# Optimization experiments

Hardware: AMD Instinct MI355X
Metric: run time of the kernel (lower is better)

## Reference

```python
import jax, jax.numpy as jnp
import numpy as np

S, B, H, NH = 2048, 4, 1024, 16
HD = H // NH
MASK_VAL = -10000.0

def setup_inputs() -> dict:
    key = jax.random.key(0)
    ks = jax.random.split(key, 6)
    hidden_states = jax.random.normal(ks[0], (S, B, H), dtype=jnp.float32)
    attention_mask = jax.random.randint(ks[1], (B, 1, S, S), 0, 2).astype(bool)
    W_qkv = jax.random.normal(ks[2], (3 * H, H), dtype=jnp.float32) * (H ** -0.5)
    b_qkv = jax.random.normal(ks[3], (3 * H,), dtype=jnp.float32) * 0.02
    W_dense = jax.random.normal(ks[4], (H, H), dtype=jnp.float32) * (H ** -0.5)
    b_dense = jax.random.normal(ks[5], (H,), dtype=jnp.float32) * 0.02
    return {"hidden_states": hidden_states, "attention_mask": attention_mask,
            "W_qkv": W_qkv, "b_qkv": b_qkv, "W_dense": W_dense, "b_dense": b_dense}

def reference(hidden_states, attention_mask, W_qkv, b_qkv, W_dense, b_dense):
    # QKV projection: [s,b,h] -> [s,b,3h] -> [s,b,NH,3*HD], split last dim into q,k,v
    mixed = hidden_states @ W_qkv.T + b_qkv
    mixed = mixed.reshape(S, B, NH, 3 * HD)
    q, k, v = mixed[..., :HD], mixed[..., HD:2 * HD], mixed[..., 2 * HD:]
    norm_factor = jnp.float32(1.0 / np.sqrt(HD))
    # scores: [b, nh, sq, sk] (baddbmm beta=0.7 on torch.empty is undefined; baseline treated as 0)
    scores = jnp.einsum('sbhd,tbhd->bhst', q, k) * norm_factor
    scores = jnp.where(attention_mask, MASK_VAL, scores)
    probs = jax.nn.softmax(scores, axis=-1)
    # attention dropout (p=0.7) omitted for deterministic reference (eval mode)
    ctx = jnp.einsum('bhst,tbhd->sbhd', probs, v)  # [s,b,nh,hd]
    ctx = ctx.reshape(S, B, H)
    out = ctx @ W_dense.T + b_dense
    return out
```

## Files before the change

### kernel.cpp

```cpp
#include <hip/hip_runtime.h>
#include <hip/hip_bf16.h>
#include <math.h>

constexpr int S_ = 2048, B_ = 4, H_ = 1024, NH_ = 16, HD_ = 64;

typedef __attribute__((ext_vector_type(8))) short short8;
typedef __attribute__((ext_vector_type(4))) short short4v;
typedef __attribute__((ext_vector_type(4))) float floatx4;
typedef __attribute__((ext_vector_type(2))) unsigned uint2v;

static __device__ __forceinline__ short f2bf(float f) {
    union { float f; unsigned u; } v; v.f = f;
    unsigned r = v.u + 0x7FFFu + ((v.u >> 16) & 1u);
    return (short)(r >> 16);
}

static __device__ __forceinline__ unsigned pack_bf(float p0, float p1) {
    return __builtin_amdgcn_perm(__float_as_uint(p1), __float_as_uint(p0), 0x07060302u);
}
static __device__ __forceinline__ float bfl(unsigned u) { return __uint_as_float(u << 16); }
static __device__ __forceinline__ float bfh(unsigned u) { return __uint_as_float(u & 0xFFFF0000u); }

static __device__ __forceinline__ void gl2lds16(const void* g, void* l) {
    __builtin_amdgcn_global_load_lds(
        (const __attribute__((address_space(1))) void*)g,
        (__attribute__((address_space(3))) void*)l, 16, 0, 0);
}

static __device__ __forceinline__ short8 pswz(unsigned a0, unsigned a1,
                                              unsigned b0, unsigned b1) {
    uint2v r0 = __builtin_amdgcn_permlane32_swap(a0, b0, false, false);
    uint2v s0 = __builtin_amdgcn_permlane16_swap(r0.x, r0.y, false, false);
    uint2v r1 = __builtin_amdgcn_permlane32_swap(a1, b1, false, false);
    uint2v s1 = __builtin_amdgcn_permlane16_swap(r1.x, r1.y, false, false);
    union { unsigned u[4]; short8 s; } o;
    o.u[0] = s0.x;
    o.u[1] = s1.x;
    o.u[2] = s0.y;
    o.u[3] = s1.y;
    return o.s;
}

__global__ __launch_bounds__(256) void cvt3_kernel(
    const float* __restrict__ a, short* __restrict__ oa, int na,
    const float* __restrict__ b, short* __restrict__ ob, int nb,
    const float* __restrict__ c, short* __restrict__ oc, int nc)
{
    const int idx = blockIdx.x * 256 + threadIdx.x;
    const float* src; short* dst; int i;
    if (idx < na)            { src = a; dst = oa; i = idx; }
    else if (idx < na + nb)  { src = b; dst = ob; i = idx - na; }
    else                     { src = c; dst = oc; i = idx - na - nb; }
    const float4 v = ((const float4*)src)[i];
    short4v o = { (short)f2bf(v.x), (short)f2bf(v.y), (short)f2bf(v.z), (short)f2bf(v.w) };
    ((short4v*)dst)[i] = o;
}

__global__ __launch_bounds__(256) void mask_u8_kernel(
    const int* __restrict__ m, unsigned* __restrict__ mb)
{
    const int i = blockIdx.x * 256 + threadIdx.x;
    const int4 v = ((const int4*)m)[i];
    unsigned r = (v.x ? 0u : 0xFFu)      | (v.y ? 0u : 0xFF00u) |
                 (v.z ? 0u : 0xFF0000u)  | (v.w ? 0u : 0xFF000000u);
    mb[i] = r;
}

__global__ __launch_bounds__(256) void gemm_qkv_mfma(
    const short* __restrict__ A, const short* __restrict__ Bw,
    const float* __restrict__ bias,
    short* __restrict__ Qb, short* __restrict__ Kb, short* __restrict__ Vb)
{
    constexpr int K = H_;
    __shared__ __align__(16) short As[128 * 64];
    __shared__ __align__(16) short Bs[128 * 64];

    const int t = threadIdx.x;
    const int wave = t >> 6, lane = t & 63;
    const int l15 = lane & 15, quad = lane >> 4;
    const int wm = wave & 1, wn = wave >> 1;
    const int row0 = blockIdx.y * 128;
    const int col0 = blockIdx.x * 128;

    floatx4 acc[4][4];
#pragma unroll
    for (int mi = 0; mi < 4; ++mi)
#pragma unroll
        for (int ni = 0; ni < 4; ++ni)
            acc[mi][ni] = (floatx4){0.f, 0.f, 0.f, 0.f};

    for (int k0 = 0; k0 < K; k0 += 64) {
#pragma unroll
        for (int j = 0; j < 4; ++j) {
            const int c = wave * 256 + j * 64 + lane;
            const int r = c >> 3, jg = ((c & 7) ^ (r & 7)) * 8;
            gl2lds16(A  + (size_t)(row0 + r) * K + k0 + jg, &As[(wave * 256 + j * 64) * 8]);
            gl2lds16(Bw + (size_t)(col0 + r) * K + k0 + jg, &Bs[(wave * 256 + j * 64) * 8]);
        }
        __syncthreads();
#pragma unroll
        for (int kk = 0; kk < 64; kk += 32) {
            short8 af[4], bfr[4];
#pragma unroll
            for (int mi = 0; mi < 4; ++mi) {
                const int R = wm * 64 + mi * 16 + l15;
                af[mi] = *(const short8*)&As[R * 64 + ((((kk >> 3) + quad) ^ (R & 7)) * 8)];
            }
#pragma unroll
            for (int ni = 0; ni < 4; ++ni) {
                const int R = wn * 64 + ni * 16 + l15;
                bfr[ni] = *(const short8*)&Bs[R * 64 + ((((kk >> 3) + quad) ^ (R & 7)) * 8)];
            }
#pragma unroll
            for (int mi = 0; mi < 4; ++mi)
#pragma unroll
                for (int ni = 0; ni < 4; ++ni)
                    acc[mi][ni] = __builtin_amdgcn_mfma_f32_16x16x32_bf16(
                        af[mi], bfr[ni], acc[mi][ni], 0, 0, 0);
        }
        __syncthreads();
    }

#pragma unroll
    for (int ni = 0; ni < 4; ++ni) {
        const int gc = col0 + wn * 64 + ni * 16 + l15;
        const float bv = bias[gc];
        const int hh = gc / 192;
        const int rem = gc - hh * 192;
        const int which = rem >> 6, d = rem & 63;
#pragma unroll
        for (int mi = 0; mi < 4; ++mi)
#pragma unroll
            for (int i = 0; i < 4; ++i) {
                const int gr = row0 + wm * 64 + mi * 16 + quad * 4 + i;
                const int s = gr >> 2, bb = gr & 3;
                float fv = acc[mi][ni][i] + bv;
                const size_t ho = (size_t)(bb * NH_ + hh);
                if (which == 0)      Qb[(ho * S_ + s) * HD_ + d] = f2bf(fv * 0.1803368801111204f);
                else if (which == 1) Kb[(ho * S_ + s) * HD_ + d] = f2bf(fv);
                else                 Vb[(ho * S_ + s) * HD_ + d] = f2bf(fv);
            }
    }
}

__global__ __launch_bounds__(256) void vtrans_kernel(
    const short* __restrict__ Vb, short* __restrict__ Vtb)
{
    const int bh = blockIdx.y;
    const int s0 = blockIdx.x * 64;
    __shared__ __align__(16) short T[64 * 64];
    const int t = threadIdx.x;

#pragma unroll
    for (int it = 0; it < 2; ++it) {
        const int c = t + it * 256;
        const int r = c >> 3, jp = c & 7;
        const int jg = jp ^ ((r >> 3) & 7);
        *(short8*)&T[r * 64 + jp * 8] =
            *(const short8*)(Vb + ((size_t)bh * S_ + s0 + r) * HD_ + jg * 8);
    }
    __syncthreads();

#pragma unroll
    for (int it = 0; it < 2; ++it) {
        const int c = t + it * 256;
        const int d = c >> 3, sg = (c & 7) * 8;
        short8 v;
#pragma unroll
        for (int k = 0; k < 8; ++k) {
            const int r = sg + k;
            v[k] = T[r * 64 + (((d >> 3) ^ ((r >> 3) & 7)) * 8) + (d & 7)];
        }
        *(short8*)(Vtb + ((size_t)bh * HD_ + d) * S_ + s0 + sg) = v;
    }
}

__global__ __launch_bounds__(256) void gemm_dense_mfma(
    const short* __restrict__ A, const short* __restrict__ Bw,
    const float* __restrict__ bias, float* __restrict__ out)
{
    constexpr int K = H_;
    __shared__ __align__(16) short As[128 * 64];
    __shared__ __align__(16) short Bs[128 * 64];

    const int t = threadIdx.x;
    const int wave = t >> 6, lane = t & 63;
    const int l15 = lane & 15, quad = lane >> 4;
    const int wm = wave & 1, wn = wave >> 1;
    const int row0 = blockIdx.y * 128;
    const int col0 = blockIdx.x * 128;

    floatx4 acc[4][4];
#pragma unroll
    for (int mi = 0; mi < 4; ++mi)
#pragma unroll
        for (int ni = 0; ni < 4; ++ni)
            acc[mi][ni] = (floatx4){0.f, 0.f, 0.f, 0.f};

    for (int k0 = 0; k0 < K; k0 += 64) {
#pragma unroll
        for (int j = 0; j < 4; ++j) {
            const int c = wave * 256 + j * 64 + lane;
            const int r = c >> 3, jg = ((c & 7) ^ (r & 7)) * 8;
            gl2lds16(A  + (size_t)(row0 + r) * K + k0 + jg, &As[(wave * 256 + j * 64) * 8]);
            gl2lds16(Bw + (size_t)(col0 + r) * K + k0 + jg, &Bs[(wave * 256 + j * 64) * 8]);
        }
        __syncthreads();
#pragma unroll
        for (int kk = 0; kk < 64; kk += 32) {
            short8 af[4], bfr[4];
#pragma unroll
            for (int mi = 0; mi < 4; ++mi) {
                const int R = wm * 64 + mi * 16 + l15;
                af[mi] = *(const short8*)&As[R * 64 + ((((kk >> 3) + quad) ^ (R & 7)) * 8)];
            }
#pragma unroll
            for (int ni = 0; ni < 4; ++ni) {
                const int R = wn * 64 + ni * 16 + l15;
                bfr[ni] = *(const short8*)&Bs[R * 64 + ((((kk >> 3) + quad) ^ (R & 7)) * 8)];
            }
#pragma unroll
            for (int mi = 0; mi < 4; ++mi)
#pragma unroll
                for (int ni = 0; ni < 4; ++ni)
                    acc[mi][ni] = __builtin_amdgcn_mfma_f32_16x16x32_bf16(
                        af[mi], bfr[ni], acc[mi][ni], 0, 0, 0);
        }
        __syncthreads();
    }

#pragma unroll
    for (int ni = 0; ni < 4; ++ni) {
        const int gc = col0 + wn * 64 + ni * 16 + l15;
        const float bv = bias[gc];
#pragma unroll
        for (int mi = 0; mi < 4; ++mi)
#pragma unroll
            for (int i = 0; i < 4; ++i) {
                const int gr = row0 + wm * 64 + mi * 16 + quad * 4 + i;
                out[(size_t)gr * H_ + gc] = acc[mi][ni][i] + bv;
            }
    }
}

__global__ __launch_bounds__(256, 2) void flash_mfma_kernel(
    const short* __restrict__ Qb, const short* __restrict__ Kb,
    const short* __restrict__ Vtb, const unsigned char* __restrict__ mask8,
    short* __restrict__ ctxb)
{
    const int bh = blockIdx.y;
    const int b  = bh >> 4;
    const int h  = bh & 15;
    const int s0 = blockIdx.x * 128;

    const int tdx  = threadIdx.x;
    const int wave = tdx >> 6;
    const int lane = tdx & 63;
    const int l15  = lane & 15;
    const int quad = lane >> 4;

    __shared__ __align__(16) short Ks [3 * 4096];
    __shared__ __align__(16) short Vts[3 * 4096];
    __shared__ __align__(16) unsigned char Ms[3 * 8192];

    const short* Qg = Qb + ((size_t)bh * S_ + s0 + wave * 32 + l15) * HD_;
    short8 qf00 = *(const short8*)(Qg + quad * 8);
    short8 qf01 = *(const short8*)(Qg + 32 + quad * 8);
    short8 qf10 = *(const short8*)(Qg + 16 * HD_ + quad * 8);
    short8 qf11 = *(const short8*)(Qg + 16 * HD_ + 32 + quad * 8);

    const short* Kbase  = Kb  + (size_t)bh * S_ * HD_;
    const short* Vtbase = Vtb + (size_t)bh * HD_ * S_;

    floatx4 o[2][4];
    float ls0 = 0.f, ls1 = 0.f;
#pragma unroll
    for (int g = 0; g < 2; ++g)
#pragma unroll
        for (int n0 = 0; n0 < 4; ++n0) o[g][n0] = (floatx4){0.f, 0.f, 0.f, 0.f};

    const int cb0 = wave * 64, cb1 = (4 + wave) * 64;
    const int c0 = cb0 + lane,  c1 = cb1 + lane;
    const int r0 = c0 >> 3, jg0 = ((c0 & 7) ^ (r0 & 7)) * 8;
    const int r1 = c1 >> 3, jg1 = ((c1 & 7) ^ (r1 & 7)) * 8;

    const int mq0 = wave * 32 + (lane >> 2);
    const int mq1 = mq0 + 16;
    const int msw0 = (mq0 & 3) ^ ((mq0 >> 2) & 3);
    const int msw1 = (mq1 & 3) ^ ((mq1 >> 2) & 3);
    const unsigned char* msrc0 = mask8 + ((size_t)b * S_ + s0 + mq0) * S_ + ((lane & 3) ^ msw0) * 16;
    const unsigned char* msrc1 = mask8 + ((size_t)b * S_ + s0 + mq1) * S_ + ((lane & 3) ^ msw1) * 16;
    const int mdst0 = wave * 2048;
    const int mdst1 = wave * 2048 + 1024;

    const int sq = (l15 & 3) ^ (l15 >> 2);
    const int mrd0 = (wave * 32 + l15) * 64 + quad * 4;
    const int mrd1 = (wave * 32 + 16 + l15) * 64 + quad * 4;

    gl2lds16(Kbase  + (size_t)r0 * HD_ + jg0, &Ks[cb0 * 8]);
    gl2lds16(Kbase  + (size_t)r1 * HD_ + jg1, &Ks[cb1 * 8]);
    gl2lds16(Vtbase + (size_t)r0 * S_ + jg0,  &Vts[cb0 * 8]);
    gl2lds16(Vtbase + (size_t)r1 * S_ + jg1,  &Vts[cb1 * 8]);
    gl2lds16(msrc0, &Ms[mdst0]);
    gl2lds16(msrc1, &Ms[mdst1]);
    __builtin_amdgcn_sched_barrier(0);
    gl2lds16(Kbase  + (size_t)(64 + r0) * HD_ + jg0, &Ks[4096 + cb0 * 8]);
    gl2lds16(Kbase  + (size_t)(64 + r1) * HD_ + jg1, &Ks[4096 + cb1 * 8]);
    gl2lds16(Vtbase + (size_t)r0 * S_ + 64 + jg0,    &Vts[4096 + cb0 * 8]);
    gl2lds16(Vtbase + (size_t)r1 * S_ + 64 + jg1,    &Vts[4096 + cb1 * 8]);
    gl2lds16(msrc0 + 64, &Ms[8192 + mdst0]);
    gl2lds16(msrc1 + 64, &Ms[8192 + mdst1]);
    __builtin_amdgcn_sched_barrier(0);

    const floatx4 z4 = {0.f, 0.f, 0.f, 0.f};
    int bc = 0, bs = 2;

#pragma unroll 1
    for (int it = 0; it < 32; ++it) {
        if (it < 31) { asm volatile("s_waitcnt vmcnt(6)" ::: "memory"); }
        else         { asm volatile("s_waitcnt vmcnt(0)" ::: "memory"); }
        __builtin_amdgcn_s_barrier();
        __builtin_amdgcn_sched_barrier(0);

        if (it < 30) {
            const size_t tn = (size_t)(it + 2) * 64;
            gl2lds16(Kbase  + (tn + r0) * HD_ + jg0,      &Ks[bs * 4096 + cb0 * 8]);
            gl2lds16(Kbase  + (tn + r1) * HD_ + jg1,      &Ks[bs * 4096 + cb1 * 8]);
            gl2lds16(Vtbase + (size_t)r0 * S_ + tn + jg0, &Vts[bs * 4096 + cb0 * 8]);
            gl2lds16(Vtbase + (size_t)r1 * S_ + tn + jg1, &Vts[bs * 4096 + cb1 * 8]);
            gl2lds16(msrc0 + tn, &Ms[bs * 8192 + mdst0]);
            gl2lds16(msrc1 + tn, &Ms[bs * 8192 + mdst1]);
        }
        __builtin_amdgcn_sched_barrier(0);

        const int bo = bc * 4096;
        const int mo = bc * 8192;
        floatx4 sc[2][4];
        __builtin_amdgcn_s_setprio(1);
#pragma unroll
        for (int n0 = 0; n0 < 4; ++n0) {
            const int R = n0 * 16 + l15, xr = R & 7;
            const short8 kb0 = *(const short8*)&Ks[bo + R * 64 + ((quad ^ xr) * 8)];
            const short8 kb1 = *(const short8*)&Ks[bo + R * 64 + (((quad + 4) ^ xr) * 8)];
            sc[0][n0] = __builtin_amdgcn_mfma_f32_16x16x32_bf16(kb0, qf00, z4, 0, 0, 0);
            sc[0][n0] = __builtin_amdgcn_mfma_f32_16x16x32_bf16(kb1, qf01, sc[0][n0], 0, 0, 0);
            sc[1][n0] = __builtin_amdgcn_mfma_f32_16x16x32_bf16(kb0, qf10, z4, 0, 0, 0);
            sc[1][n0] = __builtin_amdgcn_mfma_f32_16x16x32_bf16(kb1, qf11, sc[1][n0], 0, 0, 0);
        }
        __builtin_amdgcn_s_setprio(0);

        unsigned uu[2][4][2];
#pragma unroll
        for (int g = 0; g < 2; ++g) {
            const int mrd = g ? mrd1 : mrd0;
#pragma unroll
            for (int n0 = 0; n0 < 4; ++n0) {
                const unsigned mw = *(const unsigned*)&Ms[mo + mrd + ((n0 ^ sq) << 4)];
                const floatx4 v = sc[g][n0];
                const unsigned q0 = __builtin_amdgcn_perm(0u, mw, 0x01010000u);
                const unsigned q1 = __builtin_amdgcn_perm(0u, mw, 0x03030202u);
                const unsigned u0 = pack_bf(__builtin_amdgcn_exp2f(v[0]),
                                            __builtin_amdgcn_exp2f(v[1])) & q0;
                const unsigned u1 = pack_bf(__builtin_amdgcn_exp2f(v[2]),
                                            __builtin_amdgcn_exp2f(v[3])) & q1;
                if (g == 0) ls0 += (bfl(u0) + bfh(u0)) + (bfl(u1) + bfh(u1));
                else        ls1 += (bfl(u0) + bfh(u0)) + (bfl(u1) + bfh(u1));
                uu[g][n0][0] = u0; uu[g][n0][1] = u1;
            }
        }
        short8 pa00 = pswz(uu[0][0][0], uu[0][0][1], uu[0][1][0], uu[0][1][1]);
        short8 pa01 = pswz(uu[0][2][0], uu[0][2][1], uu[0][3][0], uu[0][3][1]);
        short8 pa10 = pswz(uu[1][0][0], uu[1][0][1], uu[1][1][0], uu[1][1][1]);
        short8 pa11 = pswz(uu[1][2][0], uu[1][2][1], uu[1][3][0], uu[1][3][1]);

        __builtin_amdgcn_s_setprio(1);
#pragma unroll
        for (int n0 = 0; n0 < 4; ++n0) {
            const int R = n0 * 16 + l15, xr = R & 7;
            const short8 vb0 = *(const short8*)&Vts[bo + R * 64 + ((quad ^ xr) * 8)];
            const short8 vb1 = *(const short8*)&Vts[bo + R * 64 + (((quad + 4) ^ xr) * 8)];
            o[0][n0] = __builtin_amdgcn_mfma_f32_16x16x32_bf16(pa00, vb0, o[0][n0], 0, 0, 0);
            o[0][n0] = __builtin_amdgcn_mfma_f32_16x16x32_bf16(pa01, vb1, o[0][n0], 0, 0, 0);
            o[1][n0] = __builtin_amdgcn_mfma_f32_16x16x32_bf16(pa10, vb0, o[1][n0], 0, 0, 0);
            o[1][n0] = __builtin_amdgcn_mfma_f32_16x16x32_bf16(pa11, vb1, o[1][n0], 0, 0, 0);
        }
        __builtin_amdgcn_s_setprio(0);

        bc = (bc == 2) ? 0 : bc + 1;
        bs = (bs == 2) ? 0 : bs + 1;
    }

#pragma unroll
    for (int g = 0; g < 2; ++g) {
        float lg = g ? ls1 : ls0;
        lg += __shfl_xor(lg, 16);
        lg += __shfl_xor(lg, 32);
        const float li = 1.f / lg;
#pragma unroll
        for (int i = 0; i < 4; ++i) {
            const float la = __shfl(li, quad * 4 + i);
            const int sA = s0 + wave * 32 + g * 16 + quad * 4 + i;
#pragma unroll
            for (int n0 = 0; n0 < 4; ++n0)
                ctxb[((size_t)sA * B_ + b) * H_ + h * HD_ + n0 * 16 + l15] =
                    f2bf(o[g][n0][i] * la);
        }
    }
}

extern "C" void kernel_launch(void* const* d_in, const int* in_sizes, int n_in,
                              void* d_out, int out_size, void* d_ws, size_t ws_size,
                              hipStream_t stream)
{
    const float* hidden = (const float*)d_in[0];
    const int*   mask   = (const int*)d_in[1];
    const float* Wqkv   = (const float*)d_in[2];
    const float* bqkv   = (const float*)d_in[3];
    const float* Wd     = (const float*)d_in[4];
    const float* bd     = (const float*)d_in[5];
    float* out = (float*)d_out;

    const size_t HE = (size_t)B_ * NH_ * S_ * HD_;
    short* hBF    = (short*)d_ws;
    short* WqkvBF = hBF + (size_t)S_ * B_ * H_;
    short* WdBF   = WqkvBF + (size_t)3 * H_ * H_;
    short* Qb     = WdBF + (size_t)H_ * H_;
    short* Kb     = Qb + HE;
    short* Vb     = Kb + HE;
    short* Vtb    = Vb + HE;
    short* ctxb   = Vtb + HE;
    unsigned char* mask8 = (unsigned char*)hBF;

    const int nh4 = (S_ * B_ * H_) / 4;
    const int nw4 = (3 * H_ * H_) / 4;
    const int nd4 = (H_ * H_) / 4;
    hipLaunchKernelGGL(cvt3_kernel, dim3((nh4 + nw4 + nd4) / 256), dim3(256), 0, stream,
                       hidden, hBF, nh4, Wqkv, WqkvBF, nw4, Wd, WdBF, nd4);

    hipLaunchKernelGGL(gemm_qkv_mfma, dim3((3 * H_) / 128, (S_ * B_) / 128), dim3(256), 0, stream,
                       hBF, WqkvBF, bqkv, Qb, Kb, Vb);
    hipLaunchKernelGGL(mask_u8_kernel, dim3((B_ * S_ * S_ / 4) / 256), dim3(256), 0, stream,
                       mask, (unsigned*)mask8);
    hipLaunchKernelGGL(vtrans_kernel, dim3(S_ / 64, B_ * NH_), dim3(256), 0, stream,
                       Vb, Vtb);
    hipLaunchKernelGGL(flash_mfma_kernel, dim3(S_ / 128, B_ * NH_), dim3(256), 0, stream,
                       Qb, Kb, Vtb, mask8, ctxb);
    hipLaunchKernelGGL(gemm_dense_mfma, dim3(H_ / 128, (S_ * B_) / 128), dim3(256), 0, stream,
                       ctxb, WdBF, bd, out);
}
```

Baseline: 363.6 us.

## Triple-buffer GEMM K-loop with async LDS loads; compute softmax row sums via MFMA

Both projection GEMMs switch from a single-buffered 64-wide K step with two full barriers per step to a 3-stage ring of 32-wide K tiles. Each tile is loaded with global_load_lds two steps ahead, guarded by explicit vmcnt waits and one barrier per step, and uses a new XOR swizzle and occupancy hint. The aim is to hide global load latency behind MFMA work. In the attention kernel, the per-lane scalar accumulation of probability row sums (unpack bf16 plus adds plus shuffles) is replaced by extra MFMAs against a ones vector, which moves that ALU work onto the matrix units.

```diff
diff --git a/kernel.cpp b/kernel.cpp
--- a/kernel.cpp
+++ b/kernel.cpp
@@ -18,8 +18,6 @@
 static __device__ __forceinline__ unsigned pack_bf(float p0, float p1) {
     return __builtin_amdgcn_perm(__float_as_uint(p1), __float_as_uint(p0), 0x07060302u);
 }
-static __device__ __forceinline__ float bfl(unsigned u) { return __uint_as_float(u << 16); }
-static __device__ __forceinline__ float bfh(unsigned u) { return __uint_as_float(u & 0xFFFF0000u); }
 
 static __device__ __forceinline__ void gl2lds16(const void* g, void* l) {
     __builtin_amdgcn_global_load_lds(
@@ -66,14 +64,14 @@
     mb[i] = r;
 }
 
-__global__ __launch_bounds__(256) void gemm_qkv_mfma(
+__global__ __launch_bounds__(256, 3) void gemm_qkv_mfma(
     const short* __restrict__ A, const short* __restrict__ Bw,
     const float* __restrict__ bias,
     short* __restrict__ Qb, short* __restrict__ Kb, short* __restrict__ Vb)
 {
     constexpr int K = H_;
-    __shared__ __align__(16) short As[128 * 64];
-    __shared__ __align__(16) short Bs[128 * 64];
+    __shared__ __align__(16) short As[3 * 4096];
+    __shared__ __align__(16) short Bs[3 * 4096];
 
     const int t = threadIdx.x;
     const int wave = t >> 6, lane = t & 63;
@@ -89,36 +87,66 @@
         for (int ni = 0; ni < 4; ++ni)
             acc[mi][ni] = (floatx4){0.f, 0.f, 0.f, 0.f};
 
-    for (int k0 = 0; k0 < K; k0 += 64) {
-#pragma unroll
-        for (int j = 0; j < 4; ++j) {
-            const int c = wave * 256 + j * 64 + lane;
-            const int r = c >> 3, jg = ((c & 7) ^ (r & 7)) * 8;
-            gl2lds16(A  + (size_t)(row0 + r) * K + k0 + jg, &As[(wave * 256 + j * 64) * 8]);
-            gl2lds16(Bw + (size_t)(col0 + r) * K + k0 + jg, &Bs[(wave * 256 + j * 64) * 8]);
-        }
-        __syncthreads();
-#pragma unroll
-        for (int kk = 0; kk < 64; kk += 32) {
-            short8 af[4], bfr[4];
-#pragma unroll
-            for (int mi = 0; mi < 4; ++mi) {
-                const int R = wm * 64 + mi * 16 + l15;
-                af[mi] = *(const short8*)&As[R * 64 + ((((kk >> 3) + quad) ^ (R & 7)) * 8)];
-            }
-#pragma unroll
-            for (int ni = 0; ni < 4; ++ni) {
-                const int R = wn * 64 + ni * 16 + l15;
-                bfr[ni] = *(const short8*)&Bs[R * 64 + ((((kk >> 3) + quad) ^ (R & 7)) * 8)];
-            }
-#pragma unroll
-            for (int mi = 0; mi < 4; ++mi)
-#pragma unroll
-                for (int ni = 0; ni < 4; ++ni)
-                    acc[mi][ni] = __builtin_amdgcn_mfma_f32_16x16x32_bf16(
-                        af[mi], bfr[ni], acc[mi][ni], 0, 0, 0);
-        }
-        __syncthreads();
+    const int c0 = wave * 128 + lane, c1 = c0 + 64;
+    const int r0 = c0 >> 2, jg0 = (((c0 & 3) ^ (((r0 & 3) + ((r0 >> 2) & 3)) & 3))) * 8;
+    const int r1 = c1 >> 2, jg1 = (((c1 & 3) ^ (((r1 & 3) + ((r1 >> 2) & 3)) & 3))) * 8;
+    const int db0 = (wave * 128) * 8;
+    const int db1 = db0 + 64 * 8;
+
+    const short* Ar0 = A  + (size_t)(row0 + r0) * K + jg0;
+    const short* Ar1 = A  + (size_t)(row0 + r1) * K + jg1;
+    const short* Br0 = Bw + (size_t)(col0 + r0) * K + jg0;
+    const short* Br1 = Bw + (size_t)(col0 + r1) * K + jg1;
+
+    gl2lds16(Ar0, &As[db0]); gl2lds16(Ar1, &As[db1]);
+    gl2lds16(Br0, &Bs[db0]); gl2lds16(Br1, &Bs[db1]);
+    __builtin_amdgcn_sched_barrier(0);
+    gl2lds16(Ar0 + 32, &As[4096 + db0]); gl2lds16(Ar1 + 32, &As[4096 + db1]);
+    gl2lds16(Br0 + 32, &Bs[4096 + db0]); gl2lds16(Br1 + 32, &Bs[4096 + db1]);
+    __builtin_amdgcn_sched_barrier(0);
+
+    int bc = 0, bs = 2;
+#pragma unroll 1
+    for (int it = 0; it < 32; ++it) {
+        if (it < 31) { asm volatile("s_waitcnt vmcnt(4)" ::: "memory"); }
+        else         { asm volatile("s_waitcnt vmcnt(0)" ::: "memory"); }
+        __builtin_amdgcn_s_barrier();
+        __builtin_amdgcn_sched_barrier(0);
+
+        if (it < 30) {
+            const int ko = (it + 2) * 32;
+            gl2lds16(Ar0 + ko, &As[bs * 4096 + db0]);
+            gl2lds16(Ar1 + ko, &As[bs * 4096 + db1]);
+            gl2lds16(Br0 + ko, &Bs[bs * 4096 + db0]);
+            gl2lds16(Br1 + ko, &Bs[bs * 4096 + db1]);
+        }
+        __builtin_amdgcn_sched_barrier(0);
+
+        const int bo = bc * 4096;
+        short8 af[4], bfr[4];
+#pragma unroll
+        for (int mi = 0; mi < 4; ++mi) {
+            const int R = wm * 64 + mi * 16 + l15;
+            const int sel = quad ^ (((R & 3) + ((R >> 2) & 3)) & 3);
+            af[mi] = *(const short8*)&As[bo + R * 32 + sel * 8];
+        }
+#pragma unroll
+        for (int ni = 0; ni < 4; ++ni) {
+            const int R = wn * 64 + ni * 16 + l15;
+            const int sel = quad ^ (((R & 3) + ((R >> 2) & 3)) & 3);
+            bfr[ni] = *(const short8*)&Bs[bo + R * 32 + sel * 8];
+        }
+        __builtin_amdgcn_s_setprio(1);
+#pragma unroll
+        for (int mi = 0; mi < 4; ++mi)
+#pragma unroll
+            for (int ni = 0; ni < 4; ++ni)
+                acc[mi][ni] = __builtin_amdgcn_mfma_f32_16x16x32_bf16(
+                    af[mi], bfr[ni], acc[mi][ni], 0, 0, 0);
+        __builtin_amdgcn_s_setprio(0);
+
+        bc = (bc == 2) ? 0 : bc + 1;
+        bs = (bs == 2) ? 0 : bs + 1;
     }
 
 #pragma unroll
@@ -175,13 +203,13 @@
     }
 }
 
-__global__ __launch_bounds__(256) void gemm_dense_mfma(
+__global__ __launch_bounds__(256, 3) void gemm_dense_mfma(
     const short* __restrict__ A, const short* __restrict__ Bw,
     const float* __restrict__ bias, float* __restrict__ out)
 {
     constexpr int K = H_;
-    __shared__ __align__(16) short As[128 * 64];
-    __shared__ __align__(16) short Bs[128 * 64];
+    __shared__ __align__(16) short As[3 * 4096];
+    __shared__ __align__(16) short Bs[3 * 4096];
 
     const int t = threadIdx.x;
     const int wave = t >> 6, lane = t & 63;
@@ -197,36 +225,66 @@
         for (int ni = 0; ni < 4; ++ni)
             acc[mi][ni] = (floatx4){0.f, 0.f, 0.f, 0.f};
 
-    for (int k0 = 0; k0 < K; k0 += 64) {
-#pragma unroll
-        for (int j = 0; j < 4; ++j) {
-            const int c = wave * 256 + j * 64 + lane;
-            const int r = c >> 3, jg = ((c & 7) ^ (r & 7)) * 8;
-            gl2lds16(A  + (size_t)(row0 + r) * K + k0 + jg, &As[(wave * 256 + j * 64) * 8]);
-            gl2lds16(Bw + (size_t)(col0 + r) * K + k0 + jg, &Bs[(wave * 256 + j * 64) * 8]);
-        }
-        __syncthreads();
-#pragma unroll
-        for (int kk = 0; kk < 64; kk += 32) {
-            short8 af[4], bfr[4];
-#pragma unroll
-            for (int mi = 0; mi < 4; ++mi) {
-                const int R = wm * 64 + mi * 16 + l15;
-                af[mi] = *(const short8*)&As[R * 64 + ((((kk >> 3) + quad) ^ (R & 7)) * 8)];
-            }
-#pragma unroll
-            for (int ni = 0; ni < 4; ++ni) {
-                const int R = wn * 64 + ni * 16 + l15;
-                bfr[ni] = *(const short8*)&Bs[R * 64 + ((((kk >> 3) + quad) ^ (R & 7)) * 8)];
-            }
-#pragma unroll
-            for (int mi = 0; mi < 4; ++mi)
-#pragma unroll
-                for (int ni = 0; ni < 4; ++ni)
-                    acc[mi][ni] = __builtin_amdgcn_mfma_f32_16x16x32_bf16(
-                        af[mi], bfr[ni], acc[mi][ni], 0, 0, 0);
-        }
-        __syncthreads();
+    const int c0 = wave * 128 + lane, c1 = c0 + 64;
+    const int r0 = c0 >> 2, jg0 = (((c0 & 3) ^ (((r0 & 3) + ((r0 >> 2) & 3)) & 3))) * 8;
+    const int r1 = c1 >> 2, jg1 = (((c1 & 3) ^ (((r1 & 3) + ((r1 >> 2) & 3)) & 3))) * 8;
+    const int db0 = (wave * 128) * 8;
+    const int db1 = db0 + 64 * 8;
+
+    const short* Ar0 = A  + (size_t)(row0 + r0) * K + jg0;
+    const short* Ar1 = A  + (size_t)(row0 + r1) * K + jg1;
+    const short* Br0 = Bw + (size_t)(col0 + r0) * K + jg0;
+    const short* Br1 = Bw + (size_t)(col0 + r1) * K + jg1;
+
+    gl2lds16(Ar0, &As[db0]); gl2lds16(Ar1, &As[db1]);
+    gl2lds16(Br0, &Bs[db0]); gl2lds16(Br1, &Bs[db1]);
+    __builtin_amdgcn_sched_barrier(0);
+    gl2lds16(Ar0 + 32, &As[4096 + db0]); gl2lds16(Ar1 + 32, &As[4096 + db1]);
+    gl2lds16(Br0 + 32, &Bs[4096 + db0]); gl2lds16(Br1 + 32, &Bs[4096 + db1]);
+    __builtin_amdgcn_sched_barrier(0);
+
+    int bc = 0, bs = 2;
+#pragma unroll 1
+    for (int it = 0; it < 32; ++it) {
+        if (it < 31) { asm volatile("s_waitcnt vmcnt(4)" ::: "memory"); }
+        else         { asm volatile("s_waitcnt vmcnt(0)" ::: "memory"); }
+        __builtin_amdgcn_s_barrier();
+        __builtin_amdgcn_sched_barrier(0);
+
+        if (it < 30) {
+            const int ko = (it + 2) * 32;
+            gl2lds16(Ar0 + ko, &As[bs * 4096 + db0]);
+            gl2lds16(Ar1 + ko, &As[bs * 4096 + db1]);
+            gl2lds16(Br0 + ko, &Bs[bs * 4096 + db0]);
+            gl2lds16(Br1 + ko, &Bs[bs * 4096 + db1]);
+        }
+        __builtin_amdgcn_sched_barrier(0);
+
+        const int bo = bc * 4096;
+        short8 af[4], bfr[4];
+#pragma unroll
+        for (int mi = 0; mi < 4; ++mi) {
+            const int R = wm * 64 + mi * 16 + l15;
+            const int sel = quad ^ (((R & 3) + ((R >> 2) & 3)) & 3);
+            af[mi] = *(const short8*)&As[bo + R * 32 + sel * 8];
+        }
+#pragma unroll
+        for (int ni = 0; ni < 4; ++ni) {
+            const int R = wn * 64 + ni * 16 + l15;
+            const int sel = quad ^ (((R & 3) + ((R >> 2) & 3)) & 3);
+            bfr[ni] = *(const short8*)&Bs[bo + R * 32 + sel * 8];
+        }
+        __builtin_amdgcn_s_setprio(1);
+#pragma unroll
+        for (int mi = 0; mi < 4; ++mi)
+#pragma unroll
+            for (int ni = 0; ni < 4; ++ni)
+                acc[mi][ni] = __builtin_amdgcn_mfma_f32_16x16x32_bf16(
+                    af[mi], bfr[ni], acc[mi][ni], 0, 0, 0);
+        __builtin_amdgcn_s_setprio(0);
+
+        bc = (bc == 2) ? 0 : bc + 1;
+        bs = (bs == 2) ? 0 : bs + 1;
     }
 
 #pragma unroll
@@ -273,11 +331,15 @@
     const short* Vtbase = Vtb + (size_t)bh * HD_ * S_;
 
     floatx4 o[2][4];
-    float ls0 = 0.f, ls1 = 0.f;
-#pragma unroll
-    for (int g = 0; g < 2; ++g)
+    floatx4 lacc[2];
+#pragma unroll
+    for (int g = 0; g < 2; ++g) {
+        lacc[g] = (floatx4){0.f, 0.f, 0.f, 0.f};
 #pragma unroll
         for (int n0 = 0; n0 < 4; ++n0) o[g][n0] = (floatx4){0.f, 0.f, 0.f, 0.f};
+    }
+    const short8 ones8 = {(short)0x3F80, (short)0x3F80, (short)0x3F80, (short)0x3F80,
+                          (short)0x3F80, (short)0x3F80, (short)0x3F80, (short)0x3F80};
 
     const int cb0 = wave * 64, cb1 = (4 + wave) * 64;
     const int c0 = cb0 + lane,  c1 = cb1 + lane;
@@ -363,8 +425,6 @@
                                             __builtin_amdgcn_exp2f(v[1])) & q0;
                 const unsigned u1 = pack_bf(__builtin_amdgcn_exp2f(v[2]),
                                             __builtin_amdgcn_exp2f(v[3])) & q1;
-                if (g == 0) ls0 += (bfl(u0) + bfh(u0)) + (bfl(u1) + bfh(u1));
-                else        ls1 += (bfl(u0) + bfh(u0)) + (bfl(u1) + bfh(u1));
                 uu[g][n0][0] = u0; uu[g][n0][1] = u1;
             }
         }
@@ -374,6 +434,10 @@
         short8 pa11 = pswz(uu[1][2][0], uu[1][2][1], uu[1][3][0], uu[1][3][1]);
 
         __builtin_amdgcn_s_setprio(1);
+        lacc[0] = __builtin_amdgcn_mfma_f32_16x16x32_bf16(pa00, ones8, lacc[0], 0, 0, 0);
+        lacc[0] = __builtin_amdgcn_mfma_f32_16x16x32_bf16(pa01, ones8, lacc[0], 0, 0, 0);
+        lacc[1] = __builtin_amdgcn_mfma_f32_16x16x32_bf16(pa10, ones8, lacc[1], 0, 0, 0);
+        lacc[1] = __builtin_amdgcn_mfma_f32_16x16x32_bf16(pa11, ones8, lacc[1], 0, 0, 0);
 #pragma unroll
         for (int n0 = 0; n0 < 4; ++n0) {
             const int R = n0 * 16 + l15, xr = R & 7;
@@ -392,13 +456,9 @@
 
 #pragma unroll
     for (int g = 0; g < 2; ++g) {
-        float lg = g ? ls1 : ls0;
-        lg += __shfl_xor(lg, 16);
-        lg += __shfl_xor(lg, 32);
-        const float li = 1.f / lg;
 #pragma unroll
         for (int i = 0; i < 4; ++i) {
-            const float la = __shfl(li, quad * 4 + i);
+            const float la = 1.f / lacc[g][i];
             const int sA = s0 + wave * 32 + g * 16 + quad * 4 + i;
 #pragma unroll
             for (int n0 = 0; n0 < 4; ++n0)
```

Result: no change. 360.1 us (-1.0%).
